# Kernel tuning notes

Measured on AMD Instinct MI355X. Metric: run time of the kernel, lower is better.

Reference implementation:

```python
import jax, jax.numpy as jnp
import numpy as np
from jax.lax import associative_scan

B, S, D, F, G = 4, 4096, 1024, 4096, 32
EPS = 1e-6


def setup_inputs() -> dict:
    key = jax.random.key(0)
    ks = jax.random.split(key, 16)
    xn = lambda k, shp: jax.random.normal(k, shp, jnp.float32) / np.sqrt(shp[0])
    return {
        "x": jax.random.normal(ks[0], (B, S, D), jnp.float32),
        "Wq": xn(ks[1], (D, D)),
        "Wk": xn(ks[2], (D, D)),
        "Wv": xn(ks[3], (D, D)),
        "Wa": xn(ks[4], (D, 2 * D)),
        "Wg": xn(ks[5], (D, D)),
        "Wo": xn(ks[6], (D, D)),
        "gn_scale": jnp.ones((D,), jnp.float32),
        "gn_bias": jnp.zeros((D,), jnp.float32),
        "ln1_scale": jnp.ones((D,), jnp.float32),
        "ln1_bias": jnp.zeros((D,), jnp.float32),
        "W1": xn(ks[7], (D, F)),
        "b1": jax.random.normal(ks[8], (F,), jnp.float32) * 1e-6,
        "W2": xn(ks[9], (F, D)),
        "b2": jax.random.normal(ks[10], (D,), jnp.float32) * 1e-6,
        "ln2_scale": jnp.ones((D,), jnp.float32),
        "ln2_bias": jnp.zeros((D,), jnp.float32),
    }


def _gate_loop(k, v, q, a):
    # max-headed GateLoop: per-channel complex linear recurrence
    # h_t = a_t * h_{t-1} + k_t * v_t ; y_t = q_t * h_t
    kv = (k * v).astype(jnp.complex64)
    def op(e1, e2):
        a1, x1 = e1
        a2, x2 = e2
        return (a1 * a2, a2 * x1 + x2)
    _, h = associative_scan(op, (a, kv), axis=1)
    return q.astype(jnp.complex64) * h


def _layernorm(x, scale, bias):
    mu = jnp.mean(x, axis=-1, keepdims=True)
    var = jnp.mean(jnp.square(x - mu), axis=-1, keepdims=True)
    return (x - mu) * jax.lax.rsqrt(var + EPS) * scale + bias


def _groupnorm_complex(y, scale, bias):
    # flax GroupNorm on complex input: mean is complex, var = E|y|^2 - |E y|^2 (real)
    b, s, d = y.shape
    yr = y.reshape(b, s, G, d // G)
    mean = jnp.mean(yr, axis=(1, 3), keepdims=True)
    mean2 = jnp.mean(yr.real ** 2 + yr.imag ** 2, axis=(1, 3), keepdims=True)
    var = mean2 - (mean.real ** 2 + mean.imag ** 2)
    yn = (yr - mean) * jax.lax.rsqrt(var + EPS)
    return yn.reshape(b, s, d) * scale + bias


def reference(x, Wq, Wk, Wv, Wa, Wg, Wo, gn_scale, gn_bias, ln1_scale, ln1_bias,
              W1, b1, W2, b2, ln2_scale, ln2_bias):
    q = x @ Wq
    k = x @ Wk
    v = x @ Wv
    a = x @ Wa
    a_real, a_imag = jnp.split(a, 2, axis=-1)
    a_c = a_real + 1j * a_imag
    mag = jnp.abs(a_c)
    phase = jnp.angle(a_c)
    a_c = jax.nn.sigmoid(mag) * jnp.exp(1j * phase)

    g = (x @ Wg).astype(jnp.complex64)

    y = _gate_loop(k, v, q, a_c)                       # [B,S,D] complex64
    y = _groupnorm_complex(y, gn_scale, gn_bias)
    silu_g = g / (1.0 + jnp.exp(-g))                    # complex silu
    y = y * silu_g
    y = (y @ Wo.astype(jnp.complex64)).real

    x = _layernorm(x + y, ln1_scale, ln1_bias)
    h = jax.nn.gelu(x @ W1 + b1)
    out = x + (h @ W2 + b2)
    return _layernorm(out, ln2_scale, ln2_bias)
```

## Files before the change

kernel.cpp:

```cpp
#include <hip/hip_runtime.h>
#include <cstdint>
#include <cstddef>


#define EPSN 1e-6f

typedef _Float16 f16;
typedef _Float16 f16x8 __attribute__((ext_vector_type(8)));
typedef _Float16 f16x4 __attribute__((ext_vector_type(4)));
typedef float    f32x4 __attribute__((ext_vector_type(4)));

static constexpr int    Bb     = 4;
static constexpr int    Ss     = 4096;
static constexpr int    Dd     = 1024;
static constexpr int    Ff     = 4096;
static constexpr int    Mrows  = Bb * Ss;
static constexpr size_t MD     = (size_t)Mrows * Dd;
static constexpr int    CHUNKS = 64;
static constexpr int    CLEN   = Ss / CHUNKS;
static constexpr int    BD     = Bb * Dd;
static constexpr int    CBD    = CHUNKS * BD;
static constexpr size_t MiB    = 1024 * 1024;
static constexpr int    PLD    = 4096;

__device__ __forceinline__ float fast_sigmoid(float x) {
    float e = __builtin_amdgcn_exp2f(-1.4426950408889634f * x);
    return __builtin_amdgcn_rcpf(1.0f + e);
}
__device__ __forceinline__ float gelu_tanh(float x) {
    float z = 0.7978845608028654f * (x + 0.044715f * x * x * x);
    z = fminf(fmaxf(z, -10.0f), 10.0f);
    float e = __builtin_amdgcn_exp2f(2.885390081777927f * z);
    float t = (e - 1.0f) * __builtin_amdgcn_rcpf(e + 1.0f);
    return 0.5f * x * (1.0f + t);
}

__device__ __forceinline__ void async16(const void* g, void* l) {
    __builtin_amdgcn_global_load_lds(
        (const __attribute__((address_space(1))) unsigned int*)(uintptr_t)g,
        (__attribute__((address_space(3))) unsigned int*)(uintptr_t)l,
        16, 0, 0);
}

template <int EPI, typename TC>
__global__ __launch_bounds__(512, 2) void mgemm_k(const f16* __restrict__ A, int lda,
                                                  const f16* __restrict__ Bt,
                                                  TC* __restrict__ C, int ldc,
                                                  int M, int N, int K,
                                                  const float* __restrict__ bias) {
    __shared__ f16 sA[4][256 * 32];
    __shared__ f16 sB[4][256 * 32];
    const int tid  = threadIdx.x;
    const int wave = tid >> 6;
    const int lane = tid & 63;

    const int gx  = gridDim.x;
    const int nwg = gx * gridDim.y;
    int bid = blockIdx.y * gx + blockIdx.x;
    bid = (bid & 7) * (nwg >> 3) + (bid >> 3);
    const int bm = (bid / gx) * 256;
    const int bn = (bid % gx) * 256;

    const int rw = (wave >> 2) * 128;
    const int cw = (wave & 3) * 64;

    const int swzc = (((lane & 3) ^ (lane >> 3)) & 3) * 8;
    const f16* gSA = A  + (size_t)(bm + wave * 32 + (lane >> 2)) * lda + swzc;
    const f16* gSB = Bt + (size_t)(bn + wave * 32 + (lane >> 2)) * K   + swzc;

    f32x4 acc[8][4] = {};

    const int fr  = lane & 15;
    const int fco = (((lane >> 4) ^ (lane >> 1)) & 3) * 8;

    const int NT = K >> 5;

#define MG_STAGE(BUF, KOFF)                                                    \
    {                                                                          \
        async16(gSA + (KOFF),                    &sA[BUF][wave * 1024]);       \
        async16(gSA + 16 * (size_t)lda + (KOFF), &sA[BUF][wave * 1024 + 512]); \
        async16(gSB + (KOFF),                    &sB[BUF][wave * 1024]);       \
        async16(gSB + 16 * (size_t)K + (KOFF),   &sB[BUF][wave * 1024 + 512]); \
    }

    MG_STAGE(0, 0)
    MG_STAGE(1, 32)
    MG_STAGE(2, 64)
    asm volatile("s_waitcnt vmcnt(8)" ::: "memory");
    __builtin_amdgcn_s_barrier();

#define MG_PHASE(T, BR)                                                        \
    {                                                                          \
        const int t_ = (T);                                                    \
        f16x8 af[8], bf[4];                                                    \
        _Pragma("unroll") for (int i = 0; i < 8; ++i)                          \
            af[i] = *(const f16x8*)&sA[BR][(rw + i * 16 + fr) * 32 + fco];     \
        _Pragma("unroll") for (int j = 0; j < 4; ++j)                          \
            bf[j] = *(const f16x8*)&sB[BR][(cw + j * 16 + fr) * 32 + fco];     \
        if (t_ + 3 < NT) {                                                     \
            MG_STAGE((BR + 3) & 3, (t_ + 3) * 32)                              \
            asm volatile("s_waitcnt vmcnt(8)" ::: "memory");                   \
        } else if (t_ + 2 < NT) {                                              \
            asm volatile("s_waitcnt vmcnt(4)" ::: "memory");                   \
        } else {                                                               \
            asm volatile("s_waitcnt vmcnt(0)" ::: "memory");                   \
        }                                                                      \
        __builtin_amdgcn_s_barrier();                                          \
        __builtin_amdgcn_s_setprio(1);                                         \
        _Pragma("unroll") for (int i = 0; i < 8; ++i)                          \
            _Pragma("unroll") for (int j = 0; j < 4; ++j)                      \
                acc[i][j] = __builtin_amdgcn_mfma_f32_16x16x32_f16(            \
                    af[i], bf[j], acc[i][j], 0, 0, 0);                         \
        __builtin_amdgcn_s_setprio(0);                                         \
        __builtin_amdgcn_s_barrier();                                          \
    }

    for (int t = 0; t + 4 <= NT; t += 4) {
        MG_PHASE(t,     0)
        MG_PHASE(t + 1, 1)
        MG_PHASE(t + 2, 2)
        MG_PHASE(t + 3, 3)
    }
#undef MG_PHASE
#undef MG_STAGE

    const int er = (lane >> 4) * 4;
    const int ec = lane & 15;
#pragma unroll
    for (int i = 0; i < 8; ++i) {
#pragma unroll
        for (int j = 0; j < 4; ++j) {
            const int col = bn + cw + j * 16 + ec;
#pragma unroll
            for (int r = 0; r < 4; ++r) {
                const size_t row = (size_t)(bm + rw + i * 16 + er + r);
                float o = acc[i][j][r];
                if (EPI == 1 || EPI == 2) o += bias[col];
                if (EPI == 1) o = gelu_tanh(o);
                if (sizeof(TC) == 4) ((float*)C)[row * ldc + col] = o;
                else                 ((f16*)C)[row * ldc + col] = (f16)o;
            }
        }
    }
}

__global__ __launch_bounds__(256) void wtrans_k(const float* __restrict__ W,
                                                f16* __restrict__ Wt,
                                                int K, int N) {
    __shared__ float t[32][33];
    const int n0 = blockIdx.x * 32, k0 = blockIdx.y * 32;
    const int tx = threadIdx.x & 31, ty = threadIdx.x >> 5;
#pragma unroll
    for (int i = 0; i < 32; i += 8)
        t[ty + i][tx] = W[(size_t)(k0 + ty + i) * N + n0 + tx];
    __syncthreads();
#pragma unroll
    for (int i = 0; i < 32; i += 8)
        Wt[(size_t)(n0 + ty + i) * K + k0 + tx] = (f16)t[tx][ty + i];
}

__global__ __launch_bounds__(256) void f2h_k(const float* __restrict__ x,
                                             f16* __restrict__ xh) {
    size_t i = ((size_t)blockIdx.x * 256 + threadIdx.x) * 4;
    float4 v = *(const float4*)&x[i];
    f16x4 s;
    s.x = (f16)v.x; s.y = (f16)v.y; s.z = (f16)v.z; s.w = (f16)v.w;
    *(f16x4*)&xh[i] = s;
}

__global__ __launch_bounds__(256) void a_transform_k(f16* __restrict__ a2d) {
    size_t gid = (size_t)blockIdx.x * 256 + threadIdx.x;
    int    j8  = (int)(gid & 127) * 8;
    size_t row = gid >> 7;
    f16x8 vr = *(f16x8*)&a2d[row * 2048 + j8];
    f16x8 vi = *(f16x8*)&a2d[row * 2048 + 1024 + j8];
#pragma unroll
    for (int i = 0; i < 8; ++i) {
        float ar = (float)vr[i], ai = (float)vi[i];
        float mag = sqrtf(ar * ar + ai * ai);
        float sg  = fast_sigmoid(mag);
        float re, im;
        if (mag > 1e-30f) { float s = sg * __builtin_amdgcn_rcpf(mag); re = ar * s; im = ai * s; }
        else              { re = sg; im = 0.0f; }
        vr[i] = (f16)re; vi[i] = (f16)im;
    }
    *(f16x8*)&a2d[row * 2048 + j8]        = vr;
    *(f16x8*)&a2d[row * 2048 + 1024 + j8] = vi;
}

__global__ __launch_bounds__(256) void scan_pass1_k(const f16* __restrict__ a2d,
                                                    const f16* __restrict__ P,
                                                    float4* __restrict__ chunk) {
    int tid = blockIdx.x * 256 + threadIdx.x;
    int d   = tid & 1023;
    int t1  = tid >> 10;
    int b   = t1 & 3;
    int c   = t1 >> 2;
    int t0  = c * CLEN;
    int rbase = b * Ss;
    float Are = 1.0f, Aim = 0.0f, Hre = 0.0f, Him = 0.0f;
    for (int t = t0; t < t0 + CLEN; ++t) {
        int r = rbase + t;
        float are = (float)a2d[(size_t)r * 2048 + d];
        float aim = (float)a2d[(size_t)r * 2048 + 1024 + d];
        float kvv = (float)P[(size_t)r * PLD + 1024 + d]
                  * (float)P[(size_t)r * PLD + 2048 + d];
        float hre = are * Hre - aim * Him + kvv;
        float him = are * Him + aim * Hre;
        Hre = hre; Him = him;
        float pre = are * Are - aim * Aim;
        float pim = are * Aim + aim * Are;
        Are = pre; Aim = pim;
    }
    chunk[tid] = make_float4(Are, Aim, Hre, Him);
}

__global__ __launch_bounds__(256) void scan_pass2_k(const float4* __restrict__ chunk,
                                                    float2* __restrict__ carry,
                                                    float* __restrict__ stats) {
    int tid = blockIdx.x * blockDim.x + threadIdx.x;
    if (tid < 512) stats[tid] = 0.0f;
    float hre = 0.0f, him = 0.0f;
    for (int c = 0; c < CHUNKS; ++c) {
        int task = c * BD + tid;
        float4 ch = chunk[task];
        carry[task] = make_float2(hre, him);
        float nre = ch.x * hre - ch.y * him + ch.z;
        float nim = ch.x * him + ch.y * hre + ch.w;
        hre = nre; him = nim;
    }
}

__global__ __launch_bounds__(256) void scan_pass3_k(const f16* __restrict__ a2d,
                                                    f16* __restrict__ P,
                                                    const float2* __restrict__ carry,
                                                    float* __restrict__ stats) {
    int tid = blockIdx.x * 256 + threadIdx.x;
    int d   = tid & 1023;
    int t1  = tid >> 10;
    int b   = t1 & 3;
    int c   = t1 >> 2;
    int t0  = c * CLEN;
    int rbase = b * Ss;
    float2 cr = carry[tid];
    float hre = cr.x, him = cr.y;
    float sre = 0.0f, sim = 0.0f, s2 = 0.0f;
    for (int t = t0; t < t0 + CLEN; ++t) {
        int r = rbase + t;
        float are = (float)a2d[(size_t)r * 2048 + d];
        float aim = (float)a2d[(size_t)r * 2048 + 1024 + d];
        float kvv = (float)P[(size_t)r * PLD + 1024 + d]
                  * (float)P[(size_t)r * PLD + 2048 + d];
        float nre = are * hre - aim * him + kvv;
        float nim = are * him + aim * hre;
        hre = nre; him = nim;
        float qv  = (float)P[(size_t)r * PLD + d];
        float yr_ = qv * hre;
        float yi_ = qv * him;
        P[(size_t)r * PLD + d] = (f16)yr_;
        sre += yr_; sim += yi_; s2 += yr_ * yr_ + yi_ * yi_;
    }
#pragma unroll
    for (int off = 16; off > 0; off >>= 1) {
        sre += __shfl_down(sre, off, 32);
        sim += __shfl_down(sim, off, 32);
        s2  += __shfl_down(s2,  off, 32);
    }
    if ((threadIdx.x & 31) == 0) {
        int idx = (b * 32 + (d >> 5)) * 4;
        atomicAdd(&stats[idx + 0], sre);
        atomicAdd(&stats[idx + 1], sim);
        atomicAdd(&stats[idx + 2], s2);
    }
}

__global__ __launch_bounds__(256) void gn_gate_k(f16* __restrict__ P,
                                                 const float* __restrict__ stats,
                                                 const float* __restrict__ gn_scale,
                                                 const float* __restrict__ gn_bias) {
    size_t gid = (size_t)blockIdx.x * 256 + threadIdx.x;
    int d8  = (int)(gid & 127) * 8;
    int row = (int)(gid >> 7);
    int b   = row >> 12;
    int grp = d8 >> 5;
    const float* st = &stats[(b * 32 + grp) * 4];
    const float invN = 1.0f / 131072.0f;
    float mre = st[0] * invN;
    float mim = st[1] * invN;
    float var = st[2] * invN - mre * mre - mim * mim;
    float rstd = rsqrtf(var + EPSN);
    f16x8 yv = *(f16x8*)&P[(size_t)row * PLD + d8];
    f16x8 gv = *(const f16x8*)&P[(size_t)row * PLD + 3072 + d8];
#pragma unroll
    for (int i = 0; i < 8; ++i) {
        float re = ((float)yv[i] - mre) * rstd * gn_scale[d8 + i] + gn_bias[d8 + i];
        float gx = (float)gv[i];
        yv[i] = (f16)(re * gx * fast_sigmoid(gx));
    }
    *(f16x8*)&P[(size_t)row * PLD + d8] = yv;
}

__device__ __forceinline__ float ldf(const float* p, size_t i) { return p[i]; }
__device__ __forceinline__ float ldf(const f16* p, size_t i)   { return (float)p[i]; }
__device__ __forceinline__ void  stf(float* p, size_t i, float v) { p[i] = v; }
__device__ __forceinline__ void  stf(f16* p, size_t i, float v)   { p[i] = (f16)v; }

__device__ __forceinline__ float block_reduce_sum(float v, float* s4, int tid) {
#pragma unroll
    for (int off = 32; off > 0; off >>= 1) v += __shfl_down(v, off, 64);
    __syncthreads();
    if ((tid & 63) == 0) s4[tid >> 6] = v;
    __syncthreads();
    return s4[0] + s4[1] + s4[2] + s4[3];
}

template <typename TA, typename TB, typename TO>
__global__ __launch_bounds__(256) void ln_k(const TA* __restrict__ a,
                                            const TB* __restrict__ b,
                                            const float* __restrict__ scale,
                                            const float* __restrict__ bias,
                                            TO* __restrict__ out) {
    __shared__ float s4[4];
    int row = blockIdx.x;
    size_t base = (size_t)row * 1024;
    int tid = threadIdx.x;
    float v[4];
    float s = 0.0f;
#pragma unroll
    for (int i = 0; i < 4; ++i) {
        int d = tid + i * 256;
        v[i] = ldf(a, base + d) + ldf(b, base + d);
        s += v[i];
    }
    float mu = block_reduce_sum(s, s4, tid) * (1.0f / 1024.0f);
    float s2 = 0.0f;
#pragma unroll
    for (int i = 0; i < 4; ++i) {
        float dv = v[i] - mu;
        s2 += dv * dv;
    }
    float var = block_reduce_sum(s2, s4, tid) * (1.0f / 1024.0f);
    float rstd = rsqrtf(var + EPSN);
#pragma unroll
    for (int i = 0; i < 4; ++i) {
        int d = tid + i * 256;
        stf(out, base + d, (v[i] - mu) * rstd * scale[d] + bias[d]);
    }
}

extern "C" void kernel_launch(void* const* d_in, const int* in_sizes, int n_in,
                              void* d_out, int out_size, void* d_ws, size_t ws_size,
                              hipStream_t stream) {
    const float* x        = (const float*)d_in[0];
    const float* Wq       = (const float*)d_in[1];
    const float* Wk       = (const float*)d_in[2];
    const float* Wv       = (const float*)d_in[3];
    const float* Wa       = (const float*)d_in[4];
    const float* Wg       = (const float*)d_in[5];
    const float* Wo       = (const float*)d_in[6];
    const float* gn_scale = (const float*)d_in[7];
    const float* gn_bias  = (const float*)d_in[8];
    const float* ln1_s    = (const float*)d_in[9];
    const float* ln1_b    = (const float*)d_in[10];
    const float* W1       = (const float*)d_in[11];
    const float* b1       = (const float*)d_in[12];
    const float* W2       = (const float*)d_in[13];
    const float* b2       = (const float*)d_in[14];
    const float* ln2_s    = (const float*)d_in[15];
    const float* ln2_b    = (const float*)d_in[16];
    float* out = (float*)d_out;

    char* base = (char*)d_ws;
    f16* W1T = (f16*)(base + 0 * MiB);
    f16* W2T = (f16*)(base + 8 * MiB);
    f16* PWT = (f16*)(base + 16 * MiB);
    f16* WoT = (f16*)(base + 24 * MiB);
    f16* WaT = (f16*)(base + 26 * MiB);
    float4* chunk = (float4*)(base + 30 * MiB);
    float2* carry = (float2*)(base + 34 * MiB);
    float*  stats = (float*)(base + 36 * MiB);
    f16* xb  = (f16*)(base + 37 * MiB);
    f16* P   = (f16*)(base + 69 * MiB);
    f16*   ab = (f16*)d_out;
    f16*   yo = (f16*)d_out;
    f16*   x1 = xb;
    f16*   h1 = P;
    float* h2 = (float*)d_out;

    dim3 blk(256);
    dim3 gblk(512);

    f2h_k<<<Mrows, blk, 0, stream>>>(x, xb);
    wtrans_k<<<dim3(128, 32), blk, 0, stream>>>(W1, W1T, Dd, Ff);
    wtrans_k<<<dim3(32, 128), blk, 0, stream>>>(W2, W2T, Ff, Dd);
    wtrans_k<<<dim3(32, 32),  blk, 0, stream>>>(Wq, PWT + 0u * 1048576, Dd, Dd);
    wtrans_k<<<dim3(32, 32),  blk, 0, stream>>>(Wk, PWT + 1u * 1048576, Dd, Dd);
    wtrans_k<<<dim3(32, 32),  blk, 0, stream>>>(Wv, PWT + 2u * 1048576, Dd, Dd);
    wtrans_k<<<dim3(32, 32),  blk, 0, stream>>>(Wg, PWT + 3u * 1048576, Dd, Dd);
    wtrans_k<<<dim3(32, 32),  blk, 0, stream>>>(Wo, WoT, Dd, Dd);
    wtrans_k<<<dim3(64, 32),  blk, 0, stream>>>(Wa, WaT, Dd, 2 * Dd);

    mgemm_k<0, f16><<<dim3(16, 64), gblk, 0, stream>>>(xb, Dd, PWT, P, PLD, Mrows, 4096, Dd, nullptr);
    mgemm_k<0, f16><<<dim3(8, 64),  gblk, 0, stream>>>(xb, Dd, WaT, ab, 2048, Mrows, 2048, Dd, nullptr);

    a_transform_k<<<MD / (256 * 8), blk, 0, stream>>>(ab);

    scan_pass1_k<<<CBD / 256, blk, 0, stream>>>(ab, P, chunk);
    scan_pass2_k<<<BD / 256, blk, 0, stream>>>(chunk, carry, stats);
    scan_pass3_k<<<CBD / 256, blk, 0, stream>>>(ab, P, carry, stats);

    gn_gate_k<<<MD / (256 * 8), blk, 0, stream>>>(P, stats, gn_scale, gn_bias);

    mgemm_k<0, f16><<<dim3(4, 64), gblk, 0, stream>>>(P, PLD, WoT, yo, Dd, Mrows, Dd, Dd, nullptr);
    ln_k<float, f16, f16><<<Mrows, blk, 0, stream>>>(x, yo, ln1_s, ln1_b, x1);

    mgemm_k<1, f16  ><<<dim3(16, 64), gblk, 0, stream>>>(x1, Dd, W1T, h1, Ff, Mrows, Ff, Dd, b1);
    mgemm_k<2, float><<<dim3(4, 64),  gblk, 0, stream>>>(h1, Ff, W2T, h2, Dd, Mrows, Dd, Ff, b2);

    ln_k<f16, float, float><<<Mrows, blk, 0, stream>>>(x1, h2, ln2_s, ln2_b, out);
}
```

Before: 918.9 us.

## Restructure GEMM mainloop to double-buffered BK=64 with quadrant-interleaved MFMA phases

Replaces the 4-stage BK=32 LDS pipeline with a 2-stage BK=64 double buffer. Each K step is split into four quadrant phases that interleave LDS fragment reads, async global-to-LDS stores and MFMA bursts, in the style of an 8-wave ping-pong schedule. The swizzle changes to an 8-way XOR over 64-wide rows. This aims to cut barrier overhead per K and hide load latency behind compute, at the cost of a shallower prefetch depth and more barriers per iteration.

```diff
diff --git a/kernel.cpp b/kernel.cpp
--- a/kernel.cpp
+++ b/kernel.cpp
@@ -48,8 +48,8 @@
                                                   TC* __restrict__ C, int ldc,
                                                   int M, int N, int K,
                                                   const float* __restrict__ bias) {
-    __shared__ f16 sA[4][256 * 32];
-    __shared__ f16 sB[4][256 * 32];
+    __shared__ f16 sA[2 * 256 * 64];
+    __shared__ f16 sB[2 * 256 * 64];
     const int tid  = threadIdx.x;
     const int wave = tid >> 6;
     const int lane = tid & 63;
@@ -64,65 +64,92 @@
     const int rw = (wave >> 2) * 128;
     const int cw = (wave & 3) * 64;
 
-    const int swzc = (((lane & 3) ^ (lane >> 3)) & 3) * 8;
-    const f16* gSA = A  + (size_t)(bm + wave * 32 + (lane >> 2)) * lda + swzc;
-    const f16* gSB = Bt + (size_t)(bn + wave * 32 + (lane >> 2)) * K   + swzc;
+    const int swz  = (((lane & 7) ^ (lane >> 3)) & 7) * 8;
+    const int srow = wave * 16 + (lane >> 3);
+    const f16* gA0 = A  + (size_t)(bm + srow) * lda + swz;
+    const f16* gB0 = Bt + (size_t)(bn + srow) * K   + swz;
 
     f32x4 acc[8][4] = {};
 
-    const int fr  = lane & 15;
-    const int fco = (((lane >> 4) ^ (lane >> 1)) & 3) * 8;
-
-    const int NT = K >> 5;
-
-#define MG_STAGE(BUF, KOFF)                                                    \
-    {                                                                          \
-        async16(gSA + (KOFF),                    &sA[BUF][wave * 1024]);       \
-        async16(gSA + 16 * (size_t)lda + (KOFF), &sA[BUF][wave * 1024 + 512]); \
-        async16(gSB + (KOFF),                    &sB[BUF][wave * 1024]);       \
-        async16(gSB + 16 * (size_t)K + (KOFF),   &sB[BUF][wave * 1024 + 512]); \
-    }
-
-    MG_STAGE(0, 0)
-    MG_STAGE(1, 32)
-    MG_STAGE(2, 64)
-    asm volatile("s_waitcnt vmcnt(8)" ::: "memory");
+    const int fr   = lane & 15;
+    const int off0 = (((lane >> 4) ^ lane) & 7) * 8;
+
+    const int NT = K >> 6;
+
+#define STG(dst, gp, ld, kOff, h, g)                                           \
+    async16((gp) + (size_t)((h) * 128 + (g) * 8) * (ld) + (kOff),              \
+            (dst) + ((h) * 128 + wave * 16 + (g) * 8) * 64)
+
+#define LDA4(ib, buf)                                                          \
+    _Pragma("unroll") for (int i = 0; i < 4; ++i) {                            \
+        const int row_ = (rw + ((ib) + i) * 16 + fr) * 64;                     \
+        a_[i][0] = *(const f16x8*)&(buf)[row_ + off0];                         \
+        a_[i][1] = *(const f16x8*)&(buf)[row_ + (off0 ^ 32)];                  \
+    }
+#define LDB2(arr, jb, buf)                                                     \
+    _Pragma("unroll") for (int j = 0; j < 2; ++j) {                            \
+        const int row_ = (cw + ((jb) + j) * 16 + fr) * 64;                     \
+        arr[j][0] = *(const f16x8*)&(buf)[row_ + off0];                        \
+        arr[j][1] = *(const f16x8*)&(buf)[row_ + (off0 ^ 32)];                 \
+    }
+#define MMQ(iq, jq, barr)                                                      \
+    __builtin_amdgcn_s_setprio(1);                                             \
+    _Pragma("unroll") for (int i = 0; i < 4; ++i)                              \
+        _Pragma("unroll") for (int j = 0; j < 2; ++j)                          \
+            _Pragma("unroll") for (int kk = 0; kk < 2; ++kk)                   \
+                acc[(iq) + i][(jq) + j] = __builtin_amdgcn_mfma_f32_16x16x32_f16( \
+                    a_[i][kk], barr[j][kk], acc[(iq) + i][(jq) + j], 0, 0, 0); \
+    __builtin_amdgcn_s_setprio(0);
+
+    STG(sA, gA0, lda, 0, 0, 0); STG(sA, gA0, lda, 0, 0, 1);
+    STG(sA, gA0, lda, 0, 1, 0); STG(sA, gA0, lda, 0, 1, 1);
+    STG(sB, gB0, K,   0, 0, 0); STG(sB, gB0, K,   0, 0, 1);
+    STG(sB, gB0, K,   0, 1, 0); STG(sB, gB0, K,   0, 1, 1);
+    asm volatile("s_waitcnt vmcnt(0)" ::: "memory");
     __builtin_amdgcn_s_barrier();
 
-#define MG_PHASE(T, BR)                                                        \
-    {                                                                          \
-        const int t_ = (T);                                                    \
-        f16x8 af[8], bf[4];                                                    \
-        _Pragma("unroll") for (int i = 0; i < 8; ++i)                          \
-            af[i] = *(const f16x8*)&sA[BR][(rw + i * 16 + fr) * 32 + fco];     \
-        _Pragma("unroll") for (int j = 0; j < 4; ++j)                          \
-            bf[j] = *(const f16x8*)&sB[BR][(cw + j * 16 + fr) * 32 + fco];     \
-        if (t_ + 3 < NT) {                                                     \
-            MG_STAGE((BR + 3) & 3, (t_ + 3) * 32)                              \
-            asm volatile("s_waitcnt vmcnt(8)" ::: "memory");                   \
-        } else if (t_ + 2 < NT) {                                              \
-            asm volatile("s_waitcnt vmcnt(4)" ::: "memory");                   \
-        } else {                                                               \
-            asm volatile("s_waitcnt vmcnt(0)" ::: "memory");                   \
-        }                                                                      \
-        __builtin_amdgcn_s_barrier();                                          \
-        __builtin_amdgcn_s_setprio(1);                                         \
-        _Pragma("unroll") for (int i = 0; i < 8; ++i)                          \
-            _Pragma("unroll") for (int j = 0; j < 4; ++j)                      \
-                acc[i][j] = __builtin_amdgcn_mfma_f32_16x16x32_f16(            \
-                    af[i], bf[j], acc[i][j], 0, 0, 0);                         \
-        __builtin_amdgcn_s_setprio(0);                                         \
-        __builtin_amdgcn_s_barrier();                                          \
-    }
-
-    for (int t = 0; t + 4 <= NT; t += 4) {
-        MG_PHASE(t,     0)
-        MG_PHASE(t + 1, 1)
-        MG_PHASE(t + 2, 2)
-        MG_PHASE(t + 3, 3)
-    }
-#undef MG_PHASE
-#undef MG_STAGE
+    for (int t = 0; t < NT; ++t) {
+        const f16* rdA = sA + (t & 1) * 16384;
+        const f16* rdB = sB + (t & 1) * 16384;
+        f16* stA = sA + ((t + 1) & 1) * 16384;
+        f16* stB = sB + ((t + 1) & 1) * 16384;
+        const int kS = (t + 1) * 64;
+        const bool doSt = (t + 1) < NT;
+        f16x8 a_[4][2], bA[2][2], bB[2][2];
+
+        LDA4(0, rdA)
+        LDB2(bA, 0, rdB)
+        if (doSt) {
+            STG(stA, gA0, lda, kS, 0, 0); STG(stA, gA0, lda, kS, 0, 1);
+            STG(stA, gA0, lda, kS, 1, 0); STG(stA, gA0, lda, kS, 1, 1);
+        }
+        __builtin_amdgcn_s_barrier();
+        MMQ(0, 0, bA)
+        __builtin_amdgcn_s_barrier();
+
+        LDB2(bB, 2, rdB)
+        if (doSt) {
+            STG(stB, gB0, K, kS, 0, 0); STG(stB, gB0, K, kS, 0, 1);
+            STG(stB, gB0, K, kS, 1, 0); STG(stB, gB0, K, kS, 1, 1);
+        }
+        __builtin_amdgcn_s_barrier();
+        MMQ(0, 2, bB)
+        __builtin_amdgcn_s_barrier();
+
+        LDA4(4, rdA)
+        __builtin_amdgcn_s_barrier();
+        MMQ(4, 2, bB)
+        __builtin_amdgcn_s_barrier();
+
+        asm volatile("s_waitcnt vmcnt(0)" ::: "memory");
+        __builtin_amdgcn_s_barrier();
+        MMQ(4, 0, bA)
+        __builtin_amdgcn_s_barrier();
+    }
+#undef STG
+#undef LDA4
+#undef LDB2
+#undef MMQ
 
     const int er = (lane >> 4) * 4;
     const int ec = lane & 15;
```

Measured after the change: 893.8 us. 1.03x faster.
